# Kernel optimization log

Measured on AMD Instinct MI355X. Metric: run time of the kernel, lower is better.

The kernel has to match this reference:

```python
import jax, jax.numpy as jnp
import numpy as np

N_LAYER = 4
N_HEAD = 12
D_MODEL = 768
SEQ_LEN = 2048
VOCAB = 50257
BATCH = 2


def _sinusoid_pe(seq_len, d_model):
    pos = np.arange(seq_len, dtype=np.float32)[:, None]
    div = np.exp(np.arange(0, d_model, 2, dtype=np.float32) * (-np.log(10000.0) / d_model))
    pe = np.zeros((seq_len, d_model), dtype=np.float32)
    pe[:, 0::2] = np.sin(pos * div)
    pe[:, 1::2] = np.cos(pos * div)
    return jnp.asarray(pe[None])  # [1, C, D]


def setup_inputs() -> dict:
    key = jax.random.key(0)
    ks = jax.random.split(key, 12)
    s = 0.02
    return {
        "features": jax.random.randint(ks[0], (BATCH, SEQ_LEN), 0, VOCAB),
        "targets": jax.random.randint(ks[1], (BATCH, SEQ_LEN), 0, VOCAB),
        "tok_embed": jax.random.normal(ks[2], (VOCAB, D_MODEL), jnp.float32) * s,
        "pos_emb": _sinusoid_pe(SEQ_LEN, D_MODEL),
        "ln1_w": jnp.ones((N_LAYER, D_MODEL), jnp.float32),
        "ln1_b": jnp.zeros((N_LAYER, D_MODEL), jnp.float32),
        "attn_w": jax.random.normal(ks[3], (N_LAYER, D_MODEL, 3 * D_MODEL), jnp.float32) * s,
        "attn_b": jnp.zeros((N_LAYER, 3 * D_MODEL), jnp.float32),
        "proj_w": jax.random.normal(ks[4], (N_LAYER, D_MODEL, D_MODEL), jnp.float32) * s,
        "proj_b": jnp.zeros((N_LAYER, D_MODEL), jnp.float32),
        "ln2_w": jnp.ones((N_LAYER, D_MODEL), jnp.float32),
        "ln2_b": jnp.zeros((N_LAYER, D_MODEL), jnp.float32),
        "ffn_w1": jax.random.normal(ks[5], (N_LAYER, D_MODEL, 4 * D_MODEL), jnp.float32) * s,
        "ffn_b1": jnp.zeros((N_LAYER, 4 * D_MODEL), jnp.float32),
        "ffn_w2": jax.random.normal(ks[6], (N_LAYER, 4 * D_MODEL, D_MODEL), jnp.float32) * s,
        "ffn_b2": jnp.zeros((N_LAYER, D_MODEL), jnp.float32),
        "lnf_w": jnp.ones((D_MODEL,), jnp.float32),
        "lnf_b": jnp.zeros((D_MODEL,), jnp.float32),
        "final_w": jax.random.normal(ks[7], (D_MODEL, VOCAB), jnp.float32) * s,
    }


def _layernorm(x, w, b, eps=1e-5):
    mu = jnp.mean(x, axis=-1, keepdims=True)
    var = jnp.var(x, axis=-1, keepdims=True)
    return (x - mu) * jax.lax.rsqrt(var + eps) * w + b


def _attention(x, wqkv, bqkv, wo, bo):
    B, C, E = x.shape
    dh = E // N_HEAD
    qkv = x @ wqkv + bqkv  # [B, C, 3E]
    q, k, v = jnp.split(qkv, 3, axis=-1)
    q = q.reshape(B, C, N_HEAD, dh)
    k = k.reshape(B, C, N_HEAD, dh)
    v = v.reshape(B, C, N_HEAD, dh)
    att = jnp.einsum("bqhd,bkhd->bhqk", q, k) / jnp.sqrt(jnp.float32(dh))
    causal = jnp.tril(jnp.ones((C, C), bool))
    att = jnp.where(causal, att, -jnp.inf)
    att = jax.nn.softmax(att, axis=-1)
    y = jnp.einsum("bhqk,bkhd->bqhd", att, v).reshape(B, C, E)
    return y @ wo + bo


def reference(features, targets, tok_embed, pos_emb, ln1_w, ln1_b, attn_w, attn_b,
              proj_w, proj_b, ln2_w, ln2_b, ffn_w1, ffn_b1, ffn_w2, ffn_b2,
              lnf_w, lnf_b, final_w):
    C = features.shape[1]
    x = tok_embed[features] + pos_emb[:, :C]
    for l in range(N_LAYER):
        h = _layernorm(x, ln1_w[l], ln1_b[l])
        x = x + _attention(h, attn_w[l], attn_b[l], proj_w[l], proj_b[l])
        h = _layernorm(x, ln2_w[l], ln2_b[l])
        h = jax.nn.gelu(h @ ffn_w1[l] + ffn_b1[l], approximate=False) @ ffn_w2[l] + ffn_b2[l]
        x = x + h
    x = _layernorm(x, lnf_w, lnf_b)
    logits = x @ final_w  # [B, C, V]
    logp = jax.nn.log_softmax(logits, axis=-1)
    tgt = targets.reshape(-1)
    valid = tgt != -1
    tgt_safe = jnp.where(valid, tgt, 0)
    nll = -jnp.take_along_axis(logp.reshape(-1, logits.shape[-1]), tgt_safe[:, None], axis=1)[:, 0]
    loss = jnp.sum(jnp.where(valid, nll, 0.0)) / jnp.maximum(jnp.sum(valid), 1)
    return logits, loss
```

## Files before the change

kernel.cpp:

```cpp
#include <hip/hip_runtime.h>
#include <math.h>

#define N_LAYER 4
#define N_HEAD  12
#define D_MODEL 768
#define SEQ     2048
#define VOCAB   50257
#define BATCH   2
#define MROWS   (BATCH*SEQ)

typedef __bf16 bf16;
typedef __bf16 bf16x8 __attribute__((ext_vector_type(8)));
typedef float  f32x4  __attribute__((ext_vector_type(4)));
typedef short  short8v __attribute__((ext_vector_type(8)));

__device__ __forceinline__ void gload16(const bf16* g, const bf16* l) {
    __builtin_amdgcn_global_load_lds(
        (const __attribute__((address_space(1))) void*)g,
        (__attribute__((address_space(3))) void*)l,
        16, 0, 0);
}

__global__ __launch_bounds__(256) void embed_kernel(
    const int* __restrict__ feat, const float* __restrict__ tok,
    const float* __restrict__ pos, float* __restrict__ x)
{
    int row = blockIdx.x;
    int cpos = row & (SEQ - 1);
    int tid = feat[row];
    const float* te = tok + (size_t)tid * D_MODEL;
    const float* pe = pos + (size_t)cpos * D_MODEL;
    float* xr = x + (size_t)row * D_MODEL;
    for (int c = threadIdx.x; c < D_MODEL; c += 256)
        xr[c] = te[c] + pe[c];
}

__global__ __launch_bounds__(256) void ln_kernel(
    const float* __restrict__ x, const float* __restrict__ w,
    const float* __restrict__ b, bf16* __restrict__ out)
{
    int row = blockIdx.x;
    const float* xr = x + (size_t)row * D_MODEL;
    float lv[3];
    float s = 0.f, ss = 0.f;
#pragma unroll
    for (int i = 0; i < 3; i++) {
        float v = xr[threadIdx.x + i * 256];
        lv[i] = v; s += v; ss += v * v;
    }
#pragma unroll
    for (int o = 32; o; o >>= 1) { s += __shfl_down(s, o, 64); ss += __shfl_down(ss, o, 64); }
    __shared__ float red[8];
    int wid = threadIdx.x >> 6;
    if ((threadIdx.x & 63) == 0) { red[wid] = s; red[wid + 4] = ss; }
    __syncthreads();
    s  = red[0] + red[1] + red[2] + red[3];
    ss = red[4] + red[5] + red[6] + red[7];
    float mu  = s * (1.f / D_MODEL);
    float var = ss * (1.f / D_MODEL) - mu * mu;
    float rs  = rsqrtf(var + 1e-5f);
#pragma unroll
    for (int i = 0; i < 3; i++) {
        int c = threadIdx.x + i * 256;
        out[(size_t)row * D_MODEL + c] = (bf16)((lv[i] - mu) * rs * w[c] + b[c]);
    }
}

__global__ __launch_bounds__(256) void transpose_conv_kernel(
    const float* __restrict__ W, bf16* __restrict__ Wt, int K, int N)
{
    int l = blockIdx.z;
    const float* Wl = W + (size_t)l * K * N;
    bf16* Wtl = Wt + (size_t)l * K * N;
    __shared__ float tile[32][33];
    int k0 = blockIdx.y * 32, n0 = blockIdx.x * 32;
    for (int idx = threadIdx.x; idx < 1024; idx += 256) {
        int i = idx >> 5, j = idx & 31;
        int n = n0 + j;
        tile[i][j] = (n < N) ? Wl[(size_t)(k0 + i) * N + n] : 0.f;
    }
    __syncthreads();
    for (int idx = threadIdx.x; idx < 1024; idx += 256) {
        int j = idx >> 5, i = idx & 31;
        int n = n0 + j;
        if (n < N) Wtl[(size_t)n * K + k0 + i] = (bf16)tile[i][j];
    }
}

__global__ __launch_bounds__(256) void vtrans_kernel(
    const bf16* __restrict__ qkv, bf16* __restrict__ vT)
{
    int j0 = blockIdx.x * 64, h = blockIdx.y, b = blockIdx.z;
    __shared__ bf16 t[64][72];
    const bf16* src = qkv + ((size_t)b * SEQ + j0) * (3 * D_MODEL) + 2 * D_MODEL + h * 64;
    int tid = threadIdx.x;
#pragma unroll
    for (int i = 0; i < 2; i++) {
        int c = tid + i * 256;
        int j = c >> 3, d8 = (c & 7) * 8;
        *(short8v*)&t[j][d8] = *(const short8v*)&src[(size_t)j * (3 * D_MODEL) + d8];
    }
    __syncthreads();
    bf16* dst = vT + ((size_t)(b * N_HEAD + h) * 64) * SEQ;
#pragma unroll
    for (int i = 0; i < 2; i++) {
        int c = tid + i * 256;
        int d = c >> 3, j8 = (c & 7) * 8;
        bf16 tmp[8];
#pragma unroll
        for (int e = 0; e < 8; e++) tmp[e] = t[j8 + e][d];
        *(short8v*)&dst[(size_t)d * SEQ + j0 + j8] = *(const short8v*)tmp;
    }
}

template<bool BIAS, bool GELU_, int OUTM, int SPLITK, bool SWZ, bool LSE>
__global__ __launch_bounds__(256) void gemm_kernel(
    const bf16* __restrict__ A, const bf16* __restrict__ Bt,
    const float* __restrict__ bias, void* __restrict__ Cout,
    float* __restrict__ rowsum,
    int M, int N, int K)
{
    __shared__ __align__(16) bf16 As[128 * 32];
    __shared__ __align__(16) bf16 Bs[128 * 32];
    int tid = threadIdx.x;
    int lane = tid & 63, wid = tid >> 6;

    int Kslice = K / SPLITK;
    int kbase = (SPLITK > 1) ? (int)blockIdx.z * Kslice : 0;

    int nbx = gridDim.x;
    int bid = blockIdx.y * nbx + blockIdx.x;
    if (SWZ) {
        int nwg = nbx * gridDim.y;
        int q = nwg >> 3, r = nwg & 7;
        int xcd = bid & 7, loc = bid >> 3;
        bid = (xcd < r ? xcd * (q + 1) : r * (q + 1) + (xcd - r) * q) + loc;
    }
    int row0 = (bid % nbx) * 128;
    int col0 = (bid / nbx) * 128;

    int wr = (wid >> 1) * 64, wc = (wid & 1) * 64;

    int srow = wid * 16 + (lane >> 2);
    int selem = (lane & 3) * 8;
    const bf16* Ab0 = A + (size_t)(row0 + srow) * K + kbase + selem;
    const bf16* Ab1 = Ab0 + (size_t)64 * K;
    int bn0 = col0 + srow;      if (bn0 >= N) bn0 = N - 1;
    int bn1 = col0 + srow + 64; if (bn1 >= N) bn1 = N - 1;
    const bf16* Bb0 = Bt + (size_t)bn0 * K + kbase + selem;
    const bf16* Bb1 = Bt + (size_t)bn1 * K + kbase + selem;
    bf16* ldsA0 = As + wid * 512;
    bf16* ldsA1 = As + (wid + 4) * 512;
    bf16* ldsB0 = Bs + wid * 512;
    bf16* ldsB1 = Bs + (wid + 4) * 512;

    f32x4 acc[4][4] = {};
    int fr = lane & 15, fg8 = (lane >> 4) * 8;

    for (int k0 = 0; k0 < Kslice; k0 += 32) {
        if (k0) __syncthreads();
        gload16(Ab0 + k0, ldsA0);
        gload16(Ab1 + k0, ldsA1);
        gload16(Bb0 + k0, ldsB0);
        gload16(Bb1 + k0, ldsB1);
        __syncthreads();

        bf16x8 af[4], bfr[4];
#pragma unroll
        for (int m = 0; m < 4; m++) af[m] = *(const bf16x8*)&As[(wr + m * 16 + fr) * 32 + fg8];
#pragma unroll
        for (int n = 0; n < 4; n++) bfr[n] = *(const bf16x8*)&Bs[(wc + n * 16 + fr) * 32 + fg8];
#pragma unroll
        for (int m = 0; m < 4; m++)
#pragma unroll
            for (int n = 0; n < 4; n++)
                acc[m][n] = __builtin_amdgcn_mfma_f32_16x16x32_bf16(af[m], bfr[n], acc[m][n], 0, 0, 0);
    }

    int g = lane >> 4;
    bool addbias = BIAS && (SPLITK == 1 || blockIdx.z == 0);
    float lsum[4][4];
    if (LSE) {
#pragma unroll
        for (int m = 0; m < 4; m++)
#pragma unroll
            for (int r = 0; r < 4; r++) lsum[m][r] = 0.f;
    }

#pragma unroll
    for (int m = 0; m < 4; m++) {
#pragma unroll
        for (int n = 0; n < 4; n++) {
            int col = col0 + wc + n * 16 + fr;
            bool ok = (col < N);
            float bv = (addbias && ok) ? bias[col] : 0.f;
#pragma unroll
            for (int r = 0; r < 4; r++) {
                int row = row0 + wr + m * 16 + g * 4 + r;
                float v = acc[m][n][r] + bv;
                if (GELU_) v = 0.5f * v * (1.f + erff(v * 0.70710678118f));
                if (ok) {
                    if (OUTM == 0)
                        ((float*)Cout)[(size_t)row * N + col] = v;
                    else if (OUTM == 1)
                        ((bf16*)Cout)[(size_t)row * N + col] = (bf16)v;
                    else if (SPLITK > 1)
                        atomicAdd(&((float*)Cout)[(size_t)row * N + col], v);
                    else
                        ((float*)Cout)[(size_t)row * N + col] += v;
                }
                if (LSE) lsum[m][r] += ok ? __expf(v) : 0.f;
            }
        }
    }

    if (LSE) {
#pragma unroll
        for (int m = 0; m < 4; m++)
#pragma unroll
            for (int r = 0; r < 4; r++) {
                float s = lsum[m][r];
#pragma unroll
                for (int o = 1; o < 16; o <<= 1) s += __shfl_xor(s, o, 64);
                lsum[m][r] = s;
            }
        if (fr == 0) {
#pragma unroll
            for (int m = 0; m < 4; m++)
#pragma unroll
                for (int r = 0; r < 4; r++)
                    atomicAdd(&rowsum[row0 + wr + m * 16 + g * 4 + r], lsum[m][r]);
        }
    }
}

__global__ __launch_bounds__(256) void attn_kernel(
    const bf16* __restrict__ qkv, const bf16* __restrict__ vT, bf16* __restrict__ y)
{
    int qt = (int)(gridDim.x - 1 - blockIdx.x), h = blockIdx.y, b = blockIdx.z;
    const size_t rs = 3 * D_MODEL;
    int tid = threadIdx.x, lane = tid & 63, wid = tid >> 6;
    int fr = lane & 15, g = lane >> 4;
    int wq = qt * 64 + wid * 16;

    const bf16* qb = qkv + (size_t)b * SEQ * rs + h * 64;
    const bf16* kb = qb + D_MODEL;
    const bf16* vb = vT + ((size_t)(b * N_HEAD + h) * 64) * SEQ;

    __shared__ bf16 Ps[4][16][72];

    bf16x8 aq[2];
#pragma unroll
    for (int kk = 0; kk < 2; kk++)
        aq[kk] = *(const bf16x8*)&qb[(size_t)(wq + fr) * rs + kk * 32 + g * 8];

    f32x4 acco[4] = {};
    float mrow[4], lrow[4];
#pragma unroll
    for (int r = 0; r < 4; r++) { mrow[r] = -1e30f; lrow[r] = 0.f; }

    int jmax = qt * 64;
    for (int j0 = 0; j0 <= jmax; j0 += 64) {
        f32x4 accs[4] = {};
#pragma unroll
        for (int n = 0; n < 4; n++)
#pragma unroll
            for (int kk = 0; kk < 2; kk++) {
                bf16x8 bk = *(const bf16x8*)&kb[(size_t)(j0 + n * 16 + fr) * rs + kk * 32 + g * 8];
                accs[n] = __builtin_amdgcn_mfma_f32_16x16x32_bf16(aq[kk], bk, accs[n], 0, 0, 0);
            }

        bool diag = (j0 == jmax);
#pragma unroll
        for (int n = 0; n < 4; n++) {
            int jc = j0 + n * 16 + fr;
#pragma unroll
            for (int r = 0; r < 4; r++) {
                float sv = accs[n][r] * 0.125f;
                if (diag) { int irow = wq + g * 4 + r; if (jc > irow) sv = -1e30f; }
                accs[n][r] = sv;
            }
        }

        float pscale[4];
#pragma unroll
        for (int r = 0; r < 4; r++) {
            float pm = fmaxf(fmaxf(accs[0][r], accs[1][r]), fmaxf(accs[2][r], accs[3][r]));
#pragma unroll
            for (int o = 1; o < 16; o <<= 1) pm = fmaxf(pm, __shfl_xor(pm, o, 64));
            float mnew = fmaxf(mrow[r], pm);
            float corr = __expf(mrow[r] - mnew);
            mrow[r] = mnew;
            float ls = 0.f;
#pragma unroll
            for (int n = 0; n < 4; n++) {
                float p = __expf(accs[n][r] - mnew);
                accs[n][r] = p; ls += p;
            }
#pragma unroll
            for (int o = 1; o < 16; o <<= 1) ls += __shfl_xor(ls, o, 64);
            lrow[r] = lrow[r] * corr + ls;
            pscale[r] = corr;
        }
#pragma unroll
        for (int n = 0; n < 4; n++)
#pragma unroll
            for (int r = 0; r < 4; r++) acco[n][r] *= pscale[r];

#pragma unroll
        for (int n = 0; n < 4; n++)
#pragma unroll
            for (int r = 0; r < 4; r++)
                Ps[wid][g * 4 + r][n * 16 + fr] = (bf16)accs[n][r];

        bf16x8 ap[2];
#pragma unroll
        for (int kk = 0; kk < 2; kk++)
            ap[kk] = *(const bf16x8*)&Ps[wid][fr][kk * 32 + g * 8];
#pragma unroll
        for (int kk = 0; kk < 2; kk++)
#pragma unroll
            for (int n = 0; n < 4; n++) {
                bf16x8 bv = *(const bf16x8*)&vb[(size_t)(n * 16 + fr) * SEQ + j0 + kk * 32 + g * 8];
                acco[n] = __builtin_amdgcn_mfma_f32_16x16x32_bf16(ap[kk], bv, acco[n], 0, 0, 0);
            }
    }

    bf16* yb = y + (size_t)b * SEQ * D_MODEL + h * 64;
#pragma unroll
    for (int n = 0; n < 4; n++)
#pragma unroll
        for (int r = 0; r < 4; r++) {
            int row = wq + g * 4 + r;
            yb[(size_t)row * D_MODEL + n * 16 + fr] = (bf16)(acco[n][r] / lrow[r]);
        }
}

__global__ __launch_bounds__(256) void loss_nll_kernel(
    const float* __restrict__ logits, const float* __restrict__ rowsum,
    const int* __restrict__ tgt, float* __restrict__ accum)
{
    int row = blockIdx.x * 256 + threadIdx.x;
    if (row >= MROWS) return;
    int t = tgt[row];
    if (t >= 0) {
        float nll = logf(rowsum[row]) - logits[(size_t)row * VOCAB + t];
        atomicAdd(accum, nll);
        atomicAdd(accum + 1, 1.f);
    }
}

__global__ void loss_final_kernel(const float* __restrict__ accum, float* __restrict__ out)
{
    out[0] = accum[0] / fmaxf(accum[1], 1.f);
}

extern "C" void kernel_launch(void* const* d_in, const int* in_sizes, int n_in,
                              void* d_out, int out_size, void* d_ws, size_t ws_size,
                              hipStream_t stream)
{
    const int*   feat  = (const int*)d_in[0];
    const int*   tgt   = (const int*)d_in[1];
    const float* tok   = (const float*)d_in[2];
    const float* pos   = (const float*)d_in[3];
    const float* ln1w  = (const float*)d_in[4];
    const float* ln1b  = (const float*)d_in[5];
    const float* attnw = (const float*)d_in[6];
    const float* attnb = (const float*)d_in[7];
    const float* projw = (const float*)d_in[8];
    const float* projb = (const float*)d_in[9];
    const float* ln2w  = (const float*)d_in[10];
    const float* ln2b  = (const float*)d_in[11];
    const float* fw1   = (const float*)d_in[12];
    const float* fb1   = (const float*)d_in[13];
    const float* fw2   = (const float*)d_in[14];
    const float* fb2   = (const float*)d_in[15];
    const float* lnfw  = (const float*)d_in[16];
    const float* lnfb  = (const float*)d_in[17];
    const float* finw  = (const float*)d_in[18];

    char* ws = (char*)d_ws;
    size_t off = 0;
    auto alloc = [&](size_t bytes) -> void* {
        void* p = ws + off; off += (bytes + 255) & ~(size_t)255; return p;
    };
    float* x     = (float*)alloc((size_t)MROWS * D_MODEL * 4);
    bf16*  h     = (bf16*) alloc((size_t)MROWS * D_MODEL * 2);
    bf16*  big   = (bf16*) alloc((size_t)MROWS * 4 * D_MODEL * 2);
    bf16*  ybuf  = (bf16*) alloc((size_t)MROWS * D_MODEL * 2);
    bf16*  vT    = (bf16*) alloc((size_t)BATCH * N_HEAD * 64 * SEQ * 2);
    bf16*  awt   = (bf16*) alloc((size_t)N_LAYER * 3 * D_MODEL * D_MODEL * 2);
    bf16*  pwt   = (bf16*) alloc((size_t)N_LAYER * D_MODEL * D_MODEL * 2);
    bf16*  f1wt  = (bf16*) alloc((size_t)N_LAYER * 4 * D_MODEL * D_MODEL * 2);
    bf16*  f2wt  = (bf16*) alloc((size_t)N_LAYER * 4 * D_MODEL * D_MODEL * 2);
    bf16*  fwt   = (bf16*) alloc((size_t)VOCAB * D_MODEL * 2);
    float* rowsum= (float*)alloc((size_t)MROWS * 4);
    float* accum = (float*)alloc(256);

    float* logits = (float*)d_out;
    float* lossp  = (float*)d_out + (size_t)MROWS * VOCAB;

    dim3 blk(256);
    transpose_conv_kernel<<<dim3(3 * D_MODEL / 32, D_MODEL / 32, N_LAYER), blk, 0, stream>>>(attnw, awt, D_MODEL, 3 * D_MODEL);
    transpose_conv_kernel<<<dim3(D_MODEL / 32, D_MODEL / 32, N_LAYER), blk, 0, stream>>>(projw, pwt, D_MODEL, D_MODEL);
    transpose_conv_kernel<<<dim3(4 * D_MODEL / 32, D_MODEL / 32, N_LAYER), blk, 0, stream>>>(fw1, f1wt, D_MODEL, 4 * D_MODEL);
    transpose_conv_kernel<<<dim3(D_MODEL / 32, 4 * D_MODEL / 32, N_LAYER), blk, 0, stream>>>(fw2, f2wt, 4 * D_MODEL, D_MODEL);
    transpose_conv_kernel<<<dim3((VOCAB + 31) / 32, D_MODEL / 32, 1), blk, 0, stream>>>(finw, fwt, D_MODEL, VOCAB);

    embed_kernel<<<MROWS, blk, 0, stream>>>(feat, tok, pos, x);

    for (int l = 0; l < N_LAYER; l++) {
        ln_kernel<<<MROWS, blk, 0, stream>>>(x, ln1w + l * D_MODEL, ln1b + l * D_MODEL, h);
        gemm_kernel<true, false, 1, 1, false, false><<<dim3(MROWS / 128, (3 * D_MODEL) / 128), blk, 0, stream>>>(
            h, awt + (size_t)l * 3 * D_MODEL * D_MODEL, attnb + l * 3 * D_MODEL, big, nullptr,
            MROWS, 3 * D_MODEL, D_MODEL);
        vtrans_kernel<<<dim3(SEQ / 64, N_HEAD, BATCH), blk, 0, stream>>>(big, vT);
        attn_kernel<<<dim3(SEQ / 64, N_HEAD, BATCH), blk, 0, stream>>>(big, vT, ybuf);
        gemm_kernel<true, false, 2, 2, false, false><<<dim3(MROWS / 128, D_MODEL / 128, 2), blk, 0, stream>>>(
            ybuf, pwt + (size_t)l * D_MODEL * D_MODEL, projb + l * D_MODEL, x, nullptr,
            MROWS, D_MODEL, D_MODEL);
        ln_kernel<<<MROWS, blk, 0, stream>>>(x, ln2w + l * D_MODEL, ln2b + l * D_MODEL, h);
        gemm_kernel<true, true, 1, 1, false, false><<<dim3(MROWS / 128, (4 * D_MODEL) / 128), blk, 0, stream>>>(
            h, f1wt + (size_t)l * 4 * D_MODEL * D_MODEL, fb1 + l * 4 * D_MODEL, big, nullptr,
            MROWS, 4 * D_MODEL, D_MODEL);
        gemm_kernel<true, false, 2, 2, false, false><<<dim3(MROWS / 128, D_MODEL / 128, 2), blk, 0, stream>>>(
            big, f2wt + (size_t)l * 4 * D_MODEL * D_MODEL, fb2 + l * D_MODEL, x, nullptr,
            MROWS, D_MODEL, 4 * D_MODEL);
    }

    ln_kernel<<<MROWS, blk, 0, stream>>>(x, lnfw, lnfb, h);

    hipMemsetAsync(rowsum, 0, (size_t)MROWS * 4, stream);
    hipMemsetAsync(accum, 0, 8, stream);

    gemm_kernel<false, false, 0, 1, true, true><<<dim3(MROWS / 128, (VOCAB + 127) / 128), blk, 0, stream>>>(
        h, fwt, nullptr, logits, rowsum, MROWS, VOCAB, D_MODEL);

    loss_nll_kernel<<<(MROWS + 255) / 256, blk, 0, stream>>>(logits, rowsum, tgt, accum);
    loss_final_kernel<<<1, 1, 0, stream>>>(accum, lossp);

    (void)in_sizes; (void)n_in; (void)out_size; (void)ws_size;
}
```

Before: 2.139 ms.

## Double-buffer GEMM LDS tiles to overlap global loads with MFMA

Splits the GEMM's shared-memory A/B tiles into two buffers and prefetches the next K-tile with global_load_lds while the current tile is being multiplied. Explicit vmcnt waits and raw s_barrier calls replace the previous load, sync and compute sequence, so memory latency can hide behind MFMA work. This doubles LDS use per block, which may lower occupancy, and depends on hand-written waitcnt counts matching the four outstanding loads.

```diff
diff --git a/kernel.cpp b/kernel.cpp
--- a/kernel.cpp
+++ b/kernel.cpp
@@ -120,8 +120,8 @@
     float* __restrict__ rowsum,
     int M, int N, int K)
 {
-    __shared__ __align__(16) bf16 As[128 * 32];
-    __shared__ __align__(16) bf16 Bs[128 * 32];
+    __shared__ __align__(16) bf16 As[2][128 * 32];
+    __shared__ __align__(16) bf16 Bs[2][128 * 32];
     int tid = threadIdx.x;
     int lane = tid & 63, wid = tid >> 6;
 
@@ -149,32 +149,44 @@
     int bn1 = col0 + srow + 64; if (bn1 >= N) bn1 = N - 1;
     const bf16* Bb0 = Bt + (size_t)bn0 * K + kbase + selem;
     const bf16* Bb1 = Bt + (size_t)bn1 * K + kbase + selem;
-    bf16* ldsA0 = As + wid * 512;
-    bf16* ldsA1 = As + (wid + 4) * 512;
-    bf16* ldsB0 = Bs + wid * 512;
-    bf16* ldsB1 = Bs + (wid + 4) * 512;
+
+    const int nt = Kslice >> 5;
+    int fr = lane & 15, fg8 = (lane >> 4) * 8;
+
+    auto stage = [&](int t, int b) {
+        int k0 = t * 32;
+        gload16(Ab0 + k0, As[b] + wid * 512);
+        gload16(Ab1 + k0, As[b] + (wid + 4) * 512);
+        gload16(Bb0 + k0, Bs[b] + wid * 512);
+        gload16(Bb1 + k0, Bs[b] + (wid + 4) * 512);
+    };
 
     f32x4 acc[4][4] = {};
-    int fr = lane & 15, fg8 = (lane >> 4) * 8;
-
-    for (int k0 = 0; k0 < Kslice; k0 += 32) {
-        if (k0) __syncthreads();
-        gload16(Ab0 + k0, ldsA0);
-        gload16(Ab1 + k0, ldsA1);
-        gload16(Bb0 + k0, ldsB0);
-        gload16(Bb1 + k0, ldsB1);
-        __syncthreads();
+    stage(0, 0);
+
+    for (int t = 0; t < nt; ++t) {
+        int cur = t & 1;
+        if (t + 1 < nt) {
+            stage(t + 1, cur ^ 1);
+            asm volatile("s_waitcnt vmcnt(4)" ::: "memory");
+        } else {
+            asm volatile("s_waitcnt vmcnt(0)" ::: "memory");
+        }
+        __builtin_amdgcn_s_barrier();
 
         bf16x8 af[4], bfr[4];
 #pragma unroll
-        for (int m = 0; m < 4; m++) af[m] = *(const bf16x8*)&As[(wr + m * 16 + fr) * 32 + fg8];
-#pragma unroll
-        for (int n = 0; n < 4; n++) bfr[n] = *(const bf16x8*)&Bs[(wc + n * 16 + fr) * 32 + fg8];
+        for (int m = 0; m < 4; m++) af[m] = *(const bf16x8*)&As[cur][(wr + m * 16 + fr) * 32 + fg8];
+#pragma unroll
+        for (int n = 0; n < 4; n++) bfr[n] = *(const bf16x8*)&Bs[cur][(wc + n * 16 + fr) * 32 + fg8];
 #pragma unroll
         for (int m = 0; m < 4; m++)
 #pragma unroll
             for (int n = 0; n < 4; n++)
                 acc[m][n] = __builtin_amdgcn_mfma_f32_16x16x32_bf16(af[m], bfr[n], acc[m][n], 0, 0, 0);
+
+        asm volatile("s_waitcnt lgkmcnt(0)" ::: "memory");
+        __builtin_amdgcn_s_barrier();
     }
 
     int g = lane >> 4;
```

After: 2.143 ms. About the same (+0.2%).
